# Kernel tuning notes

Hardware: AMD Instinct MI355X
Metric: run time of the kernel (lower is better)

Reference implementation:

```python
import jax, jax.numpy as jnp
import numpy as np

B, N, G = 16, 6000, 256
T = 200                     # TRAIN_ROIS_PER_IMAGE
RATIO = 0.33                # POSITIVE_ROI_RATIO
POS_NUM = int(T * RATIO)    # 66 positive slots
NEG_SLOTS = T - POS_NUM     # 134 negative slots
BBOX_STD = jnp.asarray([0.1, 0.1, 0.2, 0.2], jnp.float32)
EPS = 1e-8


def _rand_boxes(key, b, n):
    # valid [y1,x1,y2,x2] boxes in [0,1]
    k1, k2 = jax.random.split(key)
    tl = jax.random.uniform(k1, (b, n, 2)) * 0.7
    wh = jax.random.uniform(k2, (b, n, 2)) * 0.25 + 0.02
    return jnp.concatenate([tl, tl + wh], axis=-1).astype(jnp.float32)


def setup_inputs() -> dict:
    key = jax.random.key(0)
    k1, k2, k3, k4, k5 = jax.random.split(key, 5)
    rois = _rand_boxes(k1, B, N)
    rois = rois.at[:, N - 1000:].set(0.0)          # zero padding tail (remove_zero_padding)
    gt_boxes = _rand_boxes(k2, B, G)
    gt_ids = jax.random.randint(k3, (B, G), 1, 81, dtype=jnp.int32)
    gt_ids = gt_ids.at[:, G - 32:G - 16].set(-1)   # crowd boxes (ids < 0)
    gt_ids = gt_ids.at[:, G - 16:].set(0)          # padded gt
    gt_boxes = gt_boxes.at[:, G - 16:].set(0.0)
    pos_score = jax.random.uniform(k4, (B, N), dtype=jnp.float32)
    neg_score = jax.random.uniform(k5, (B, N), dtype=jnp.float32)
    return {"rois": rois, "gt_ids": gt_ids, "gt_boxes": gt_boxes,
            "pos_score": pos_score, "neg_score": neg_score}


def _pairwise_iou(a, b):
    # a:[N,4], b:[G,4] -> [N,G]
    y1 = jnp.maximum(a[:, None, 0], b[None, :, 0])
    x1 = jnp.maximum(a[:, None, 1], b[None, :, 1])
    y2 = jnp.minimum(a[:, None, 2], b[None, :, 2])
    x2 = jnp.minimum(a[:, None, 3], b[None, :, 3])
    inter = jnp.clip(y2 - y1, 0.0) * jnp.clip(x2 - x1, 0.0)
    area_a = (a[:, 2] - a[:, 0]) * (a[:, 3] - a[:, 1])
    area_b = (b[:, 2] - b[:, 0]) * (b[:, 3] - b[:, 1])
    union = area_a[:, None] + area_b[None, :] - inter
    return inter / jnp.maximum(union, EPS)


def _bbox_offset(boxes, gt):
    h = jnp.maximum(boxes[:, 2] - boxes[:, 0], EPS)
    w = jnp.maximum(boxes[:, 3] - boxes[:, 1], EPS)
    cy = boxes[:, 0] + 0.5 * h
    cx = boxes[:, 1] + 0.5 * w
    gh = jnp.maximum(gt[:, 2] - gt[:, 0], EPS)
    gw = jnp.maximum(gt[:, 3] - gt[:, 1], EPS)
    gcy = gt[:, 0] + 0.5 * gh
    gcx = gt[:, 1] + 0.5 * gw
    off = jnp.stack([(gcy - cy) / h, (gcx - cx) / w,
                     jnp.log(gh / h), jnp.log(gw / w)], axis=1)
    return off / BBOX_STD


def _per_image(rois, gt_ids, gt_boxes, pos_score, neg_score):
    roi_valid = jnp.any(rois != 0.0, axis=1)        # [N]
    gt_valid = jnp.any(gt_boxes != 0.0, axis=1)     # [G]
    crowd = gt_valid & (gt_ids < 0)
    non_crowd = gt_valid & (gt_ids > 0)

    iou = _pairwise_iou(rois, gt_boxes)             # [N,G]
    iou_nc = jnp.where(non_crowd[None, :], iou, -1.0)
    iou_nc_max = jnp.max(iou_nc, axis=1)
    iou_cr_max = jnp.max(jnp.where(crowd[None, :], iou, 0.0), axis=1)

    pos_mask = roi_valid & (iou_nc_max >= 0.5)
    neg_mask = roi_valid & (iou_nc_max < 0.5) & (iou_cr_max < 0.001)

    # random sampling == sort by iid uniform scores (masked out -> -inf)
    pos_idx = jnp.argsort(-jnp.where(pos_mask, pos_score, -jnp.inf))[:POS_NUM]
    pos_count = jnp.minimum(jnp.sum(pos_mask), POS_NUM).astype(jnp.int32)
    pos_slot_valid = jnp.arange(POS_NUM) < pos_count

    neg_target = (jnp.float32(1.0 / RATIO) * pos_count.astype(jnp.float32)).astype(jnp.int32) - pos_count
    neg_idx = jnp.argsort(-jnp.where(neg_mask, neg_score, -jnp.inf))[:NEG_SLOTS]
    neg_count = jnp.minimum(jnp.sum(neg_mask).astype(jnp.int32),
                            jnp.minimum(neg_target, NEG_SLOTS))
    neg_slot_valid = jnp.arange(NEG_SLOTS) < neg_count

    pos_rois_raw = rois[pos_idx]                                   # [P,4]
    pos_rois = jnp.where(pos_slot_valid[:, None], pos_rois_raw, 0.0)
    neg_rois = jnp.where(neg_slot_valid[:, None], rois[neg_idx], 0.0)

    assign = jnp.argmax(iou_nc[pos_idx], axis=1)                   # gt assignment
    roi_gt_boxes = gt_boxes[assign]
    roi_gt_ids = jnp.where(pos_slot_valid, gt_ids[assign], 0)

    off = _bbox_offset(pos_rois_raw, roi_gt_boxes)
    off = jnp.where(pos_slot_valid[:, None], off, 0.0)

    out_rois = jnp.concatenate([pos_rois, neg_rois], axis=0)       # [T,4]
    out_ids = jnp.pad(roi_gt_ids, (0, NEG_SLOTS))                  # [T]
    out_off = jnp.pad(off, ((0, NEG_SLOTS), (0, 0)))               # [T,4]
    return out_rois, out_ids, out_off


def reference(rois, gt_ids, gt_boxes, pos_score, neg_score):
    return jax.vmap(_per_image)(rois, gt_ids, gt_boxes, pos_score, neg_score)
```

## Files before the change

kernel.cpp:

```cpp
#include <hip/hip_runtime.h>

#define BIMG 16
#define NROI 6000
#define NGT  256
#define TPOS 66
#define TNEG 134
#define TTOT 200
#define EPSF 1e-8f

typedef unsigned long long u64;
typedef unsigned int u32;

__global__ void pack_gt_kernel(const int* __restrict__ gt_ids,
                               const float* __restrict__ gt_boxes,
                               float* __restrict__ gt_pack)
{
#pragma clang fp contract(off)
    const int b = blockIdx.x;
    const int g = threadIdx.x;
    float4 gb = ((const float4*)gt_boxes)[b * NGT + g];
    float area = (gb.z - gb.x) * (gb.w - gb.y);
    bool valid = (gb.x != 0.f) || (gb.y != 0.f) || (gb.z != 0.f) || (gb.w != 0.f);
    int id = gt_ids[b * NGT + g];
    float flag = valid ? (id > 0 ? 1.f : (id < 0 ? 2.f : 0.f)) : 0.f;
    float4* dst = (float4*)(gt_pack + (size_t)(b * NGT + g) * 8);
    dst[0] = gb;
    dst[1] = make_float4(area, flag, 0.f, 0.f);
}

__global__ __launch_bounds__(256)
void iou_keys_kernel(const float* __restrict__ rois,
                     const float* __restrict__ gt_pack,
                     const float* __restrict__ pos_score,
                     const float* __restrict__ neg_score,
                     u64* __restrict__ pos_key,
                     u64* __restrict__ neg_key,
                     unsigned char* __restrict__ assign)
{
#pragma clang fp contract(off)
    const int b = blockIdx.y;
    __shared__ float4 s_pack[NGT * 2];
    {
        const float4* gp = (const float4*)(gt_pack + (size_t)b * NGT * 8);
        s_pack[threadIdx.x] = gp[threadIdx.x];
        s_pack[threadIdx.x + 256] = gp[threadIdx.x + 256];
    }
    __syncthreads();

    const int r_local = threadIdx.x >> 2;
    const int sub = threadIdx.x & 3;
    const int n = blockIdx.x * 64 + r_local;
    const int n_eff = min(n, NROI - 1);

    float4 rb = ((const float4*)rois)[b * NROI + n_eff];
    const bool rvalid = (rb.x != 0.f) || (rb.y != 0.f) || (rb.z != 0.f) || (rb.w != 0.f);
    const float area_a = (rb.z - rb.x) * (rb.w - rb.y);

    float best = -1.0f;
    int bestg = sub * 64;
    float crmax = 0.0f;

    const int g0 = sub * 64;
    for (int gg = 0; gg < 64; ++gg) {
        int g = g0 + gg;
        float4 p0 = s_pack[g * 2];
        float4 p1 = s_pack[g * 2 + 1];
        float y1 = fmaxf(rb.x, p0.x);
        float x1 = fmaxf(rb.y, p0.y);
        float y2 = fminf(rb.z, p0.z);
        float x2 = fminf(rb.w, p0.w);
        float ih = fmaxf(y2 - y1, 0.0f);
        float iw = fmaxf(x2 - x1, 0.0f);
        float inter = ih * iw;
        float uni = fmaxf(area_a + p1.x - inter, EPSF);
        float iou = inter / uni;
        float vnc = (p1.y == 1.f) ? iou : -1.0f;
        if (vnc > best) { best = vnc; bestg = g; }
        float vcr = (p1.y == 2.f) ? iou : 0.0f;
        crmax = fmaxf(crmax, vcr);
    }

    for (int m = 1; m <= 2; m <<= 1) {
        float ov = __shfl_xor(best, m);
        int   og = __shfl_xor(bestg, m);
        float oc = __shfl_xor(crmax, m);
        if (ov > best || (ov == best && og < bestg)) { best = ov; bestg = og; }
        crmax = fmaxf(crmax, oc);
    }

    if (sub == 0 && n < NROI) {
        u64 pk = 0ull, nk = 0ull;
        if (rvalid) {
            if (best >= 0.5f) {
                u32 sb = __float_as_uint(pos_score[b * NROI + n]);
                pk = ((u64)sb << 32) | (u32)(~n);
            }
            if ((best < 0.5f) && (crmax < 0.001f)) {
                u32 sb = __float_as_uint(neg_score[b * NROI + n]);
                nk = ((u64)sb << 32) | (u32)(~n);
            }
        }
        pos_key[b * NROI + n] = pk;
        neg_key[b * NROI + n] = nk;
        assign[b * NROI + n] = (unsigned char)bestg;
    }
}

#define BSEL 1024
#define SLOTS 6
__global__ __launch_bounds__(BSEL)
void select_kernel(const u64* __restrict__ pos_key,
                   const u64* __restrict__ neg_key,
                   int* __restrict__ sel,
                   int* __restrict__ counts)
{
    __shared__ u32 s_hist[16][256];
    __shared__ u32 s_tot[256];
    __shared__ u32 s_sufl[64];
    __shared__ u64 s_comp[TNEG];
    __shared__ int s_cnt;
    __shared__ int s_count;
    __shared__ int s_pick;
    __shared__ u32 s_higher;

    const int b = blockIdx.x >> 1;
    const int which = blockIdx.x & 1;
    const int K = which ? TNEG : TPOS;
    const u64* src = (which ? neg_key : pos_key) + (size_t)b * NROI;
    const int tid = threadIdx.x;
    const int wid = tid >> 6;

    u64 key[SLOTS];
    int myvalid = 0;
    for (int s = 0; s < SLOTS; ++s) {
        int idx = s * BSEL + tid;
        key[s] = (idx < NROI) ? src[idx] : 0ull;
        myvalid += (key[s] != 0ull);
    }

    for (int off = 1; off < 64; off <<= 1) myvalid += __shfl_xor(myvalid, off);
    if (tid == 0) s_count = 0;
    __syncthreads();
    if ((tid & 63) == 0) atomicAdd(&s_count, myvalid);
    __syncthreads();
    const int count = s_count;
    if (tid == 0) counts[b * 2 + which] = count;

    if (count > 0) {
        int Krem = min(K, count);
        u64 prefix = 0ull, mask = 0ull;

        for (int p = 7; p >= 0; --p) {
            const int shift = p * 8;
            for (int i = tid; i < 16 * 256; i += BSEL) ((u32*)s_hist)[i] = 0;
            __syncthreads();
            for (int s = 0; s < SLOTS; ++s) {
                u64 k = key[s];
                if ((k & mask) == prefix) {
                    u32 byte = (u32)(k >> shift) & 255u;
                    atomicAdd(&s_hist[wid][byte], 1u);
                }
            }
            __syncthreads();
            if (tid < 256) {
                u32 t = 0;
                for (int w = 0; w < 16; ++w) t += s_hist[w][tid];
                s_tot[tid] = t;
            }
            __syncthreads();
            if (tid < 64) {
                int l = tid;
                u32 x = s_tot[4 * l] + s_tot[4 * l + 1] + s_tot[4 * l + 2] + s_tot[4 * l + 3];
                u32 suf = x;
                for (int off = 1; off < 64; off <<= 1) {
                    u32 v = __shfl_down(suf, off);
                    if (l + off < 64) suf += v;
                }
                s_sufl[l] = suf;
            }
            __syncthreads();
            if (tid < 256) {
                int l = tid >> 2;
                u32 suffix = s_sufl[l];
                for (int j = 4 * l; j < tid; ++j) suffix -= s_tot[j];
                u32 sufnext = suffix - s_tot[tid];
                if (suffix >= (u32)Krem && sufnext < (u32)Krem) {
                    s_pick = tid;
                    s_higher = sufnext;
                }
            }
            __syncthreads();
            prefix |= ((u64)(u32)s_pick) << shift;
            mask |= (0xFFull << shift);
            Krem -= (int)s_higher;
            __syncthreads();
        }
        if (tid == 0) s_cnt = 0;
        __syncthreads();
        for (int s = 0; s < SLOTS; ++s) {
            u64 k = key[s];
            if (k >= prefix) {
                int pos = atomicAdd(&s_cnt, 1);
                s_comp[pos] = k;
            }
        }
        __syncthreads();
        const int Ksel = s_cnt;
        if (tid < Ksel) {
            u64 k = s_comp[tid];
            int rank = 0;
            for (int j = 0; j < Ksel; ++j) rank += (s_comp[j] > k);
            int n = (int)(~(u32)(k & 0xFFFFFFFFull));
            sel[(b * 2 + which) * TNEG + rank] = n;
        }
    }
}

__global__ void gather_kernel(const float* __restrict__ rois,
                              const int* __restrict__ gt_ids,
                              const float* __restrict__ gt_boxes,
                              const int* __restrict__ sel,
                              const int* __restrict__ counts,
                              const unsigned char* __restrict__ assign,
                              float* __restrict__ out)
{
#pragma clang fp contract(off)
    const int b = blockIdx.x;
    const int t = threadIdx.x;
    if (t >= TTOT) return;

    const int pos_total = counts[b * 2 + 0];
    const int neg_total = counts[b * 2 + 1];
    const int pos_count = min(pos_total, TPOS);
    const float ratio_inv = (float)(1.0 / 0.33);
    const int neg_target = (int)(ratio_inv * (float)pos_count) - pos_count;
    const int neg_count = min(neg_total, min(neg_target, TNEG));

    float* out_rois = out;
    float* out_ids  = out + BIMG * TTOT * 4;
    float* out_off  = out + BIMG * TTOT * 4 + BIMG * TTOT;

    const int base = b * TTOT + t;
    float4 ro  = make_float4(0.f, 0.f, 0.f, 0.f);
    float  idv = 0.f;
    float4 off = make_float4(0.f, 0.f, 0.f, 0.f);

    if (t < TPOS) {
        if (t < pos_count) {
            int n = sel[(b * 2 + 0) * TNEG + t];
            float4 rb = ((const float4*)rois)[b * NROI + n];
            ro = rb;
            int g = (int)assign[b * NROI + n];
            float4 gb = ((const float4*)gt_boxes)[b * NGT + g];
            idv = (float)gt_ids[b * NGT + g];

            float h  = fmaxf(rb.z - rb.x, EPSF);
            float w  = fmaxf(rb.w - rb.y, EPSF);
            float cy = rb.x + 0.5f * h;
            float cx = rb.y + 0.5f * w;
            float gh = fmaxf(gb.z - gb.x, EPSF);
            float gw = fmaxf(gb.w - gb.y, EPSF);
            float gcy = gb.x + 0.5f * gh;
            float gcx = gb.y + 0.5f * gw;
            off.x = ((gcy - cy) / h) / 0.1f;
            off.y = ((gcx - cx) / w) / 0.1f;
            off.z = logf(gh / h) / 0.2f;
            off.w = logf(gw / w) / 0.2f;
        }
    } else {
        int q = t - TPOS;
        if (q < neg_count) {
            int n = sel[(b * 2 + 1) * TNEG + q];
            ro = ((const float4*)rois)[b * NROI + n];
        }
    }

    ((float4*)out_rois)[base] = ro;
    out_ids[base] = idv;
    ((float4*)out_off)[base] = off;
}

extern "C" void kernel_launch(void* const* d_in, const int* in_sizes, int n_in,
                              void* d_out, int out_size, void* d_ws, size_t ws_size,
                              hipStream_t stream) {
    const float* rois      = (const float*)d_in[0];
    const int*   gt_ids    = (const int*)d_in[1];
    const float* gt_boxes  = (const float*)d_in[2];
    const float* pos_score = (const float*)d_in[3];
    const float* neg_score = (const float*)d_in[4];
    float* out = (float*)d_out;

    char* ws = (char*)d_ws;
    u64* pos_key = (u64*)(ws + 0);
    u64* neg_key = (u64*)(ws + 768000);
    float* gt_pack = (float*)(ws + 1536000);
    unsigned char* assign = (unsigned char*)(ws + 1667072);
    int* counts = (int*)(ws + 1763072);
    int* sel    = (int*)(ws + 1763200);

    pack_gt_kernel<<<BIMG, NGT, 0, stream>>>(gt_ids, gt_boxes, gt_pack);
    dim3 gridA((NROI + 63) / 64, BIMG);
    iou_keys_kernel<<<gridA, 256, 0, stream>>>(rois, gt_pack, pos_score, neg_score,
                                               pos_key, neg_key, assign);
    select_kernel<<<BIMG * 2, BSEL, 0, stream>>>(pos_key, neg_key, sel, counts);
    gather_kernel<<<BIMG, 256, 0, stream>>>(rois, gt_ids, gt_boxes,
                                            sel, counts, assign, out);
}
```

Before: 110.4 us.

## Fuse GT packing into IoU kernel and merge selection with gather

Drops the separate GT packing kernel: each IoU block now builds its own shared-memory box and area/flag tables. The IoU split changes to 8 lanes per ROI with interleaved GT indexing. Keys become 32-bit scores, and selection is a 4-pass 11-bit radix select with a single histogram. Positive selection, negative selection (with K sized from the positive count) and the output gather run in one block per image. This removes two launches and halves key traffic, but the fused kernel runs only 16 blocks and does pos then neg serially.

```diff
diff --git a/kernel.cpp b/kernel.cpp
--- a/kernel.cpp
+++ b/kernel.cpp
@@ -7,49 +7,41 @@
 #define TNEG 134
 #define TTOT 200
 #define EPSF 1e-8f
+#define INVALID_SCORE 0xFFFFFFFFu
 
 typedef unsigned long long u64;
 typedef unsigned int u32;
-
-__global__ void pack_gt_kernel(const int* __restrict__ gt_ids,
-                               const float* __restrict__ gt_boxes,
-                               float* __restrict__ gt_pack)
-{
-#pragma clang fp contract(off)
-    const int b = blockIdx.x;
-    const int g = threadIdx.x;
-    float4 gb = ((const float4*)gt_boxes)[b * NGT + g];
-    float area = (gb.z - gb.x) * (gb.w - gb.y);
-    bool valid = (gb.x != 0.f) || (gb.y != 0.f) || (gb.z != 0.f) || (gb.w != 0.f);
-    int id = gt_ids[b * NGT + g];
-    float flag = valid ? (id > 0 ? 1.f : (id < 0 ? 2.f : 0.f)) : 0.f;
-    float4* dst = (float4*)(gt_pack + (size_t)(b * NGT + g) * 8);
-    dst[0] = gb;
-    dst[1] = make_float4(area, flag, 0.f, 0.f);
-}
+typedef unsigned char u8;
 
 __global__ __launch_bounds__(256)
 void iou_keys_kernel(const float* __restrict__ rois,
-                     const float* __restrict__ gt_pack,
+                     const int* __restrict__ gt_ids,
+                     const float* __restrict__ gt_boxes,
                      const float* __restrict__ pos_score,
                      const float* __restrict__ neg_score,
-                     u64* __restrict__ pos_key,
-                     u64* __restrict__ neg_key,
-                     unsigned char* __restrict__ assign)
+                     u32* __restrict__ pos_s,
+                     u32* __restrict__ neg_s,
+                     u8* __restrict__ assign)
 {
 #pragma clang fp contract(off)
     const int b = blockIdx.y;
-    __shared__ float4 s_pack[NGT * 2];
+    __shared__ float4 s_box[NGT];
+    __shared__ float2 s_af[NGT];
     {
-        const float4* gp = (const float4*)(gt_pack + (size_t)b * NGT * 8);
-        s_pack[threadIdx.x] = gp[threadIdx.x];
-        s_pack[threadIdx.x + 256] = gp[threadIdx.x + 256];
-    }
-    __syncthreads();
-
-    const int r_local = threadIdx.x >> 2;
-    const int sub = threadIdx.x & 3;
-    const int n = blockIdx.x * 64 + r_local;
+        const int g = threadIdx.x;
+        float4 gb = ((const float4*)gt_boxes)[b * NGT + g];
+        s_box[g] = gb;
+        float area = (gb.z - gb.x) * (gb.w - gb.y);
+        bool valid = (gb.x != 0.f) || (gb.y != 0.f) || (gb.z != 0.f) || (gb.w != 0.f);
+        int id = gt_ids[b * NGT + g];
+        float flag = valid ? (id > 0 ? 1.f : (id < 0 ? 2.f : 0.f)) : 0.f;
+        s_af[g] = make_float2(area, flag);
+    }
+    __syncthreads();
+
+    const int r_local = threadIdx.x >> 3;
+    const int sub = threadIdx.x & 7;
+    const int n = blockIdx.x * 32 + r_local;
     const int n_eff = min(n, NROI - 1);
 
     float4 rb = ((const float4*)rois)[b * NROI + n_eff];
@@ -57,14 +49,13 @@
     const float area_a = (rb.z - rb.x) * (rb.w - rb.y);
 
     float best = -1.0f;
-    int bestg = sub * 64;
+    int bestg = sub;
     float crmax = 0.0f;
 
-    const int g0 = sub * 64;
-    for (int gg = 0; gg < 64; ++gg) {
-        int g = g0 + gg;
-        float4 p0 = s_pack[g * 2];
-        float4 p1 = s_pack[g * 2 + 1];
+    for (int gg = 0; gg < 32; ++gg) {
+        const int g = (gg << 3) | sub;
+        float4 p0 = s_box[g];
+        float2 af = s_af[g];
         float y1 = fmaxf(rb.x, p0.x);
         float x1 = fmaxf(rb.y, p0.y);
         float y2 = fminf(rb.z, p0.z);
@@ -72,15 +63,15 @@
         float ih = fmaxf(y2 - y1, 0.0f);
         float iw = fmaxf(x2 - x1, 0.0f);
         float inter = ih * iw;
-        float uni = fmaxf(area_a + p1.x - inter, EPSF);
+        float uni = fmaxf(area_a + af.x - inter, EPSF);
         float iou = inter / uni;
-        float vnc = (p1.y == 1.f) ? iou : -1.0f;
+        float vnc = (af.y == 1.f) ? iou : -1.0f;
         if (vnc > best) { best = vnc; bestg = g; }
-        float vcr = (p1.y == 2.f) ? iou : 0.0f;
+        float vcr = (af.y == 2.f) ? iou : 0.0f;
         crmax = fmaxf(crmax, vcr);
     }
 
-    for (int m = 1; m <= 2; m <<= 1) {
+    for (int m = 1; m <= 4; m <<= 1) {
         float ov = __shfl_xor(best, m);
         int   og = __shfl_xor(bestg, m);
         float oc = __shfl_xor(crmax, m);
@@ -89,195 +80,197 @@
     }
 
     if (sub == 0 && n < NROI) {
-        u64 pk = 0ull, nk = 0ull;
+        u32 ps = INVALID_SCORE, ns = INVALID_SCORE;
         if (rvalid) {
-            if (best >= 0.5f) {
-                u32 sb = __float_as_uint(pos_score[b * NROI + n]);
-                pk = ((u64)sb << 32) | (u32)(~n);
-            }
-            if ((best < 0.5f) && (crmax < 0.001f)) {
-                u32 sb = __float_as_uint(neg_score[b * NROI + n]);
-                nk = ((u64)sb << 32) | (u32)(~n);
-            }
-        }
-        pos_key[b * NROI + n] = pk;
-        neg_key[b * NROI + n] = nk;
-        assign[b * NROI + n] = (unsigned char)bestg;
-    }
-}
-
-#define BSEL 1024
-#define SLOTS 6
-__global__ __launch_bounds__(BSEL)
-void select_kernel(const u64* __restrict__ pos_key,
-                   const u64* __restrict__ neg_key,
-                   int* __restrict__ sel,
-                   int* __restrict__ counts)
+            if (best >= 0.5f)
+                ps = __float_as_uint(pos_score[b * NROI + n]);
+            if ((best < 0.5f) && (crmax < 0.001f))
+                ns = __float_as_uint(neg_score[b * NROI + n]);
+        }
+        pos_s[b * NROI + n] = ps;
+        neg_s[b * NROI + n] = ns;
+        assign[b * NROI + n] = (u8)bestg;
+    }
+}
+
+#define BSEL 512
+#define SLOTS 12
+
+__device__ __forceinline__ int radix_select(const u32* __restrict__ src, int K,
+                                            int tid, int lane, int w,
+                                            u32* s_hist, u32* s_wtot, u32* s_wsuf,
+                                            int* s_pick, u32* s_higher,
+                                            int* s_count, u64* s_comp, int* s_cnt,
+                                            int* s_sel )
 {
-    __shared__ u32 s_hist[16][256];
-    __shared__ u32 s_tot[256];
-    __shared__ u32 s_sufl[64];
-    __shared__ u64 s_comp[TNEG];
-    __shared__ int s_cnt;
-    __shared__ int s_count;
-    __shared__ int s_pick;
-    __shared__ u32 s_higher;
-
-    const int b = blockIdx.x >> 1;
-    const int which = blockIdx.x & 1;
-    const int K = which ? TNEG : TPOS;
-    const u64* src = (which ? neg_key : pos_key) + (size_t)b * NROI;
-    const int tid = threadIdx.x;
-    const int wid = tid >> 6;
-
-    u64 key[SLOTS];
+    u32 sc[SLOTS];
     int myvalid = 0;
     for (int s = 0; s < SLOTS; ++s) {
         int idx = s * BSEL + tid;
-        key[s] = (idx < NROI) ? src[idx] : 0ull;
-        myvalid += (key[s] != 0ull);
-    }
-
+        sc[s] = (idx < NROI) ? src[idx] : INVALID_SCORE;
+        myvalid += (sc[s] != INVALID_SCORE);
+    }
     for (int off = 1; off < 64; off <<= 1) myvalid += __shfl_xor(myvalid, off);
-    if (tid == 0) s_count = 0;
-    __syncthreads();
-    if ((tid & 63) == 0) atomicAdd(&s_count, myvalid);
-    __syncthreads();
-    const int count = s_count;
-    if (tid == 0) counts[b * 2 + which] = count;
-
-    if (count > 0) {
-        int Krem = min(K, count);
-        u64 prefix = 0ull, mask = 0ull;
-
-        for (int p = 7; p >= 0; --p) {
-            const int shift = p * 8;
-            for (int i = tid; i < 16 * 256; i += BSEL) ((u32*)s_hist)[i] = 0;
-            __syncthreads();
-            for (int s = 0; s < SLOTS; ++s) {
-                u64 k = key[s];
-                if ((k & mask) == prefix) {
-                    u32 byte = (u32)(k >> shift) & 255u;
-                    atomicAdd(&s_hist[wid][byte], 1u);
-                }
-            }
-            __syncthreads();
-            if (tid < 256) {
-                u32 t = 0;
-                for (int w = 0; w < 16; ++w) t += s_hist[w][tid];
-                s_tot[tid] = t;
-            }
-            __syncthreads();
-            if (tid < 64) {
-                int l = tid;
-                u32 x = s_tot[4 * l] + s_tot[4 * l + 1] + s_tot[4 * l + 2] + s_tot[4 * l + 3];
-                u32 suf = x;
-                for (int off = 1; off < 64; off <<= 1) {
-                    u32 v = __shfl_down(suf, off);
-                    if (l + off < 64) suf += v;
-                }
-                s_sufl[l] = suf;
-            }
-            __syncthreads();
-            if (tid < 256) {
-                int l = tid >> 2;
-                u32 suffix = s_sufl[l];
-                for (int j = 4 * l; j < tid; ++j) suffix -= s_tot[j];
-                u32 sufnext = suffix - s_tot[tid];
-                if (suffix >= (u32)Krem && sufnext < (u32)Krem) {
-                    s_pick = tid;
-                    s_higher = sufnext;
-                }
-            }
-            __syncthreads();
-            prefix |= ((u64)(u32)s_pick) << shift;
-            mask |= (0xFFull << shift);
-            Krem -= (int)s_higher;
-            __syncthreads();
-        }
-        if (tid == 0) s_cnt = 0;
+    if (tid == 0) *s_count = 0;
+    __syncthreads();
+    if (lane == 0) atomicAdd(s_count, (u32)myvalid);
+    __syncthreads();
+    const int total = *s_count;
+    int Krem = min(K, total);
+    if (Krem <= 0) return total;
+
+    u64 prefix = 0ull, mask = 0ull;
+    for (int p = 3; p >= 0; --p) {
+        const int shift = p * 11;
+        for (int i = tid; i < 2048; i += BSEL) s_hist[i] = 0;
         __syncthreads();
         for (int s = 0; s < SLOTS; ++s) {
-            u64 k = key[s];
+            if (sc[s] != INVALID_SCORE) {
+                u64 k = ((u64)sc[s] << 13) | (u64)(8191 - (s * BSEL + tid));
+                if ((k & mask) == prefix)
+                    atomicAdd(&s_hist[(u32)(k >> shift) & 2047u], 1u);
+            }
+        }
+        __syncthreads();
+        u32 local = s_hist[4 * tid] + s_hist[4 * tid + 1]
+                  + s_hist[4 * tid + 2] + s_hist[4 * tid + 3];
+        u32 suf = local;
+        for (int off = 1; off < 64; off <<= 1) {
+            u32 v = __shfl_down(suf, off);
+            if (lane + off < 64) suf += v;
+        }
+        if (lane == 0) s_wtot[w] = suf;
+        __syncthreads();
+        if (tid < 8) {
+            u32 t = 0;
+            for (int j = tid + 1; j < 8; ++j) t += s_wtot[j];
+            s_wsuf[tid] = t;
+        }
+        __syncthreads();
+        u32 Sincl = suf + s_wsuf[w];
+        for (int k2 = 0; k2 < 4; ++k2) {
+            u32 h = s_hist[4 * tid + k2];
+            u32 Snext = Sincl - h;
+            if (Sincl >= (u32)Krem && Snext < (u32)Krem) {
+                *s_pick = 4 * tid + k2;
+                *s_higher = Snext;
+            }
+            Sincl = Snext;
+        }
+        __syncthreads();
+        prefix |= ((u64)(u32)(*s_pick)) << shift;
+        mask   |= (2047ull << shift);
+        Krem   -= (int)(*s_higher);
+        __syncthreads();
+    }
+    if (tid == 0) *s_cnt = 0;
+    __syncthreads();
+    for (int s = 0; s < SLOTS; ++s) {
+        if (sc[s] != INVALID_SCORE) {
+            u64 k = ((u64)sc[s] << 13) | (u64)(8191 - (s * BSEL + tid));
             if (k >= prefix) {
-                int pos = atomicAdd(&s_cnt, 1);
+                int pos = atomicAdd(s_cnt, 1);
                 s_comp[pos] = k;
             }
         }
-        __syncthreads();
-        const int Ksel = s_cnt;
-        if (tid < Ksel) {
-            u64 k = s_comp[tid];
-            int rank = 0;
-            for (int j = 0; j < Ksel; ++j) rank += (s_comp[j] > k);
-            int n = (int)(~(u32)(k & 0xFFFFFFFFull));
-            sel[(b * 2 + which) * TNEG + rank] = n;
-        }
-    }
-}
-
-__global__ void gather_kernel(const float* __restrict__ rois,
-                              const int* __restrict__ gt_ids,
-                              const float* __restrict__ gt_boxes,
-                              const int* __restrict__ sel,
-                              const int* __restrict__ counts,
-                              const unsigned char* __restrict__ assign,
-                              float* __restrict__ out)
+    }
+    __syncthreads();
+    const int Ksel = *s_cnt;
+    if (tid < Ksel) {
+        u64 k = s_comp[tid];
+        int rank = 0;
+        for (int j = 0; j < Ksel; ++j) rank += (s_comp[j] > k);
+        s_sel[rank] = 8191 - (int)(k & 8191ull);
+    }
+    __syncthreads();
+    return total;
+}
+
+__global__ __launch_bounds__(BSEL)
+void select_gather_kernel(const float* __restrict__ rois,
+                          const int* __restrict__ gt_ids,
+                          const float* __restrict__ gt_boxes,
+                          const u32* __restrict__ pos_s,
+                          const u32* __restrict__ neg_s,
+                          const u8* __restrict__ assign,
+                          float* __restrict__ out)
 {
 #pragma clang fp contract(off)
+    __shared__ u32 s_hist[2048];
+    __shared__ u32 s_wtot[8];
+    __shared__ u32 s_wsuf[8];
+    __shared__ int s_pick;
+    __shared__ u32 s_higher;
+    __shared__ int s_count;
+    __shared__ u64 s_comp[TNEG];
+    __shared__ int s_cnt;
+    __shared__ int s_selpos[TPOS];
+    __shared__ int s_selneg[TNEG];
+
     const int b = blockIdx.x;
-    const int t = threadIdx.x;
-    if (t >= TTOT) return;
-
-    const int pos_total = counts[b * 2 + 0];
-    const int neg_total = counts[b * 2 + 1];
+    const int tid = threadIdx.x;
+    const int lane = tid & 63;
+    const int w = tid >> 6;
+
+    const int pos_total = radix_select(pos_s + (size_t)b * NROI, TPOS, tid, lane, w,
+                                       s_hist, s_wtot, s_wsuf, &s_pick, &s_higher,
+                                       &s_count, s_comp, &s_cnt, s_selpos);
     const int pos_count = min(pos_total, TPOS);
     const float ratio_inv = (float)(1.0 / 0.33);
     const int neg_target = (int)(ratio_inv * (float)pos_count) - pos_count;
-    const int neg_count = min(neg_total, min(neg_target, TNEG));
-
-    float* out_rois = out;
-    float* out_ids  = out + BIMG * TTOT * 4;
-    float* out_off  = out + BIMG * TTOT * 4 + BIMG * TTOT;
-
-    const int base = b * TTOT + t;
-    float4 ro  = make_float4(0.f, 0.f, 0.f, 0.f);
-    float  idv = 0.f;
-    float4 off = make_float4(0.f, 0.f, 0.f, 0.f);
-
-    if (t < TPOS) {
-        if (t < pos_count) {
-            int n = sel[(b * 2 + 0) * TNEG + t];
-            float4 rb = ((const float4*)rois)[b * NROI + n];
-            ro = rb;
-            int g = (int)assign[b * NROI + n];
-            float4 gb = ((const float4*)gt_boxes)[b * NGT + g];
-            idv = (float)gt_ids[b * NGT + g];
-
-            float h  = fmaxf(rb.z - rb.x, EPSF);
-            float w  = fmaxf(rb.w - rb.y, EPSF);
-            float cy = rb.x + 0.5f * h;
-            float cx = rb.y + 0.5f * w;
-            float gh = fmaxf(gb.z - gb.x, EPSF);
-            float gw = fmaxf(gb.w - gb.y, EPSF);
-            float gcy = gb.x + 0.5f * gh;
-            float gcx = gb.y + 0.5f * gw;
-            off.x = ((gcy - cy) / h) / 0.1f;
-            off.y = ((gcx - cx) / w) / 0.1f;
-            off.z = logf(gh / h) / 0.2f;
-            off.w = logf(gw / w) / 0.2f;
-        }
-    } else {
-        int q = t - TPOS;
-        if (q < neg_count) {
-            int n = sel[(b * 2 + 1) * TNEG + q];
-            ro = ((const float4*)rois)[b * NROI + n];
-        }
-    }
-
-    ((float4*)out_rois)[base] = ro;
-    out_ids[base] = idv;
-    ((float4*)out_off)[base] = off;
+    const int Kneg = min(neg_target, TNEG);
+    int neg_count = 0;
+    if (Kneg > 0) {
+        const int neg_total = radix_select(neg_s + (size_t)b * NROI, Kneg, tid, lane, w,
+                                           s_hist, s_wtot, s_wsuf, &s_pick, &s_higher,
+                                           &s_count, s_comp, &s_cnt, s_selneg);
+        neg_count = min(neg_total, Kneg);
+    }
+
+    if (tid < TTOT) {
+        float* out_rois = out;
+        float* out_ids  = out + BIMG * TTOT * 4;
+        float* out_off  = out + BIMG * TTOT * 4 + BIMG * TTOT;
+        const int base = b * TTOT + tid;
+
+        float4 ro  = make_float4(0.f, 0.f, 0.f, 0.f);
+        float  idv = 0.f;
+        float4 off = make_float4(0.f, 0.f, 0.f, 0.f);
+
+        if (tid < TPOS) {
+            if (tid < pos_count) {
+                int n = s_selpos[tid];
+                float4 rb = ((const float4*)rois)[b * NROI + n];
+                ro = rb;
+                int g = (int)assign[b * NROI + n];
+                float4 gb = ((const float4*)gt_boxes)[b * NGT + g];
+                idv = (float)gt_ids[b * NGT + g];
+
+                float h  = fmaxf(rb.z - rb.x, EPSF);
+                float wd = fmaxf(rb.w - rb.y, EPSF);
+                float cy = rb.x + 0.5f * h;
+                float cx = rb.y + 0.5f * wd;
+                float gh = fmaxf(gb.z - gb.x, EPSF);
+                float gw = fmaxf(gb.w - gb.y, EPSF);
+                float gcy = gb.x + 0.5f * gh;
+                float gcx = gb.y + 0.5f * gw;
+                off.x = ((gcy - cy) / h)  / 0.1f;
+                off.y = ((gcx - cx) / wd) / 0.1f;
+                off.z = logf(gh / h)  / 0.2f;
+                off.w = logf(gw / wd) / 0.2f;
+            }
+        } else {
+            int q = tid - TPOS;
+            if (q < neg_count) {
+                int n = s_selneg[q];
+                ro = ((const float4*)rois)[b * NROI + n];
+            }
+        }
+
+        ((float4*)out_rois)[base] = ro;
+        out_ids[base] = idv;
+        ((float4*)out_off)[base] = off;
+    }
 }
 
 extern "C" void kernel_launch(void* const* d_in, const int* in_sizes, int n_in,
@@ -291,18 +284,14 @@
     float* out = (float*)d_out;
 
     char* ws = (char*)d_ws;
-    u64* pos_key = (u64*)(ws + 0);
-    u64* neg_key = (u64*)(ws + 768000);
-    float* gt_pack = (float*)(ws + 1536000);
-    unsigned char* assign = (unsigned char*)(ws + 1667072);
-    int* counts = (int*)(ws + 1763072);
-    int* sel    = (int*)(ws + 1763200);
-
-    pack_gt_kernel<<<BIMG, NGT, 0, stream>>>(gt_ids, gt_boxes, gt_pack);
-    dim3 gridA((NROI + 63) / 64, BIMG);
-    iou_keys_kernel<<<gridA, 256, 0, stream>>>(rois, gt_pack, pos_score, neg_score,
-                                               pos_key, neg_key, assign);
-    select_kernel<<<BIMG * 2, BSEL, 0, stream>>>(pos_key, neg_key, sel, counts);
-    gather_kernel<<<BIMG, 256, 0, stream>>>(rois, gt_ids, gt_boxes,
-                                            sel, counts, assign, out);
-}
+    u32* pos_s = (u32*)(ws + 0);
+    u32* neg_s = (u32*)(ws + 384000);
+    u8*  assign = (u8*)(ws + 768000);
+
+    dim3 gridA((NROI + 31) / 32, BIMG);
+    iou_keys_kernel<<<gridA, 256, 0, stream>>>(rois, gt_ids, gt_boxes,
+                                               pos_score, neg_score,
+                                               pos_s, neg_s, assign);
+    select_gather_kernel<<<BIMG, BSEL, 0, stream>>>(rois, gt_ids, gt_boxes,
+                                                    pos_s, neg_s, assign, out);
+}
```

Measured after the change: 105.8 us. 4.2% less time.
